# Kernel tuning notes

Hardware: AMD Instinct MI355X
Metric: run time of the kernel (lower is better)

## Reference

```python
import jax, jax.numpy as jnp
import numpy as np

N_NODES = 100000
N_EDGES = 3200000
IN_DIM = 256
HID_DIM = 64
OUT_DIM = 64


def setup_inputs() -> dict:
    key = jax.random.key(0)
    k1, k2, k3, k4, k5, k6 = jax.random.split(key, 6)
    x = jax.random.normal(k1, (N_NODES, IN_DIM), dtype=jnp.float32)
    edge_index = jax.random.randint(k2, (2, N_EDGES), 0, N_NODES, dtype=jnp.int32)
    # Glorot-style init for the two GCNConv layers (PyG default: glorot weight, zero bias)
    W1 = jax.random.normal(k3, (IN_DIM, HID_DIM), dtype=jnp.float32) * (1.0 / np.sqrt(IN_DIM))
    b1 = jnp.zeros((HID_DIM,), dtype=jnp.float32)
    W2 = jax.random.normal(k4, (HID_DIM, OUT_DIM), dtype=jnp.float32) * (1.0 / np.sqrt(HID_DIM))
    b2 = jnp.zeros((OUT_DIM,), dtype=jnp.float32)
    return {"x": x, "edge_index": edge_index, "W1": W1, "b1": b1, "W2": W2, "b2": b2}


def _gcn_conv(x, src, dst, deg_inv_sqrt, W, b, n):
    # PyG GCNConv: h = x W; out_i = sum_j norm_ij * h_j + b, with symmetric norm
    h = x @ W                                   # (n, d_out) small GEMM
    norm = deg_inv_sqrt[src] * deg_inv_sqrt[dst]  # (E+n,)
    msg = norm[:, None] * h[src]                # gather (E+n, d_out)
    agg = jax.ops.segment_sum(msg, dst, num_segments=n)  # scatter-add
    return agg + b


def reference(x, edge_index, W1, b1, W2, b2):
    n = x.shape[0]
    loops = jnp.arange(n, dtype=edge_index.dtype)
    src = jnp.concatenate([edge_index[0], loops])
    dst = jnp.concatenate([edge_index[1], loops])
    # degree on destination (col) with added self-loops, weight 1.0
    deg = jax.ops.segment_sum(jnp.ones_like(dst, dtype=x.dtype), dst, num_segments=n)
    deg_inv_sqrt = jnp.where(deg > 0, jax.lax.rsqrt(deg), 0.0)
    h = jax.nn.relu(_gcn_conv(x, src, dst, deg_inv_sqrt, W1, b1, n))
    return _gcn_conv(h, src, dst, deg_inv_sqrt, W2, b2, n)
```

## Files before the change

kernel.cpp:

```cpp
#include <hip/hip_runtime.h>
#include <cstdint>
#include <cstddef>


#define BIN_SHIFT 7
#define BIN_NODES 128
#define MAX_BINS 1024
#define SUP_SHIFT 11
#define FINE_PER_SUP 16
#define NSUP_MAX 64
#define SCAP 56
#define SRC_BITS 17
#define SRC_MASK ((1 << SRC_BITS) - 1)

typedef unsigned short ushort_t;

typedef __attribute__((ext_vector_type(8))) short bf16x8;
typedef __attribute__((ext_vector_type(4))) float f32x4;

union FragB {
  uint4 u;
  bf16x8 b;
};

__device__ __forceinline__ float4 bfq2f4(uint2 p) {
  float4 r;
  r.x = __uint_as_float(p.x << 16);
  r.y = __uint_as_float(p.x & 0xFFFF0000u);
  r.z = __uint_as_float(p.y << 16);
  r.w = __uint_as_float(p.y & 0xFFFF0000u);
  return r;
}
__device__ __forceinline__ unsigned f2bf(float f) {
  unsigned u = __float_as_uint(f);
  return (u + 0x7FFFu + ((u >> 16) & 1u)) >> 16;
}
__device__ __forceinline__ uint2 f42bfq(float4 f) {
  uint2 r;
  r.x = f2bf(f.x) | (f2bf(f.y) << 16);
  r.y = f2bf(f.z) | (f2bf(f.w) << 16);
  return r;
}

__global__ void zero_int(int* __restrict__ p, int n) {
  int i = blockIdx.x * blockDim.x + threadIdx.x;
  if (i < n) p[i] = 0;
}

__global__ __launch_bounds__(256) void bin_count(const int* __restrict__ dst, int E, int nbins,
                                                 int* __restrict__ binCnt) {
  __shared__ int h[MAX_BINS];
  for (int i = threadIdx.x; i < nbins; i += 256) h[i] = 0;
  __syncthreads();
  int stride = gridDim.x * 256;
  for (int e = blockIdx.x * 256 + threadIdx.x; e < E; e += stride)
    atomicAdd(&h[dst[e] >> BIN_SHIFT], 1);
  __syncthreads();
  for (int i = threadIdx.x; i < nbins; i += 256)
    if (h[i]) atomicAdd(&binCnt[i], h[i]);
}

__global__ __launch_bounds__(256) void bin_scan(const int* __restrict__ binCnt, int nbins, int E,
                                                int* __restrict__ binStart,
                                                int* __restrict__ binCursor,
                                                int* __restrict__ supCursor) {
  __shared__ int s[256];
  int t = threadIdx.x;
  int c[4];
  int sum = 0;
#pragma unroll
  for (int i = 0; i < 4; i++) {
    int idx = t * 4 + i;
    c[i] = (idx < nbins) ? binCnt[idx] : 0;
    sum += c[i];
  }
  int v = sum;
  s[t] = v;
  __syncthreads();
  for (int d = 1; d < 256; d <<= 1) {
    int add = (t >= d) ? s[t - d] : 0;
    __syncthreads();
    s[t] += add;
    __syncthreads();
  }
  int run = s[t] - v;
#pragma unroll
  for (int i = 0; i < 4; i++) {
    int idx = t * 4 + i;
    if (idx < nbins) {
      binStart[idx] = run;
      binCursor[idx] = run;
      if ((idx & (FINE_PER_SUP - 1)) == 0) supCursor[idx >> 4] = run;
      run += c[i];
    }
  }
  if (t == 0) binStart[nbins] = E;
}

__global__ __launch_bounds__(256) void super_fill(const int* __restrict__ src,
                                                  const int* __restrict__ dst, int E, int nsup,
                                                  int* __restrict__ supCursor,
                                                  unsigned* __restrict__ supbuf) {
  __shared__ unsigned stage[NSUP_MAX * SCAP];
  __shared__ int lcnt[NSUP_MAX], lbase[NSUP_MAX], lscan[NSUP_MAX + 1];
  const int tid = threadIdx.x;
  const int t0 = blockIdx.x * 2048;
  const int t1 = min(E, t0 + 2048);

  int dv[8], sv[8];
#pragma unroll
  for (int i = 0; i < 8; i++) {
    int e = t0 + i * 256 + tid;
    if (e < t1) {
      dv[i] = dst[e];
      sv[i] = src[e];
    }
  }
  if (tid < nsup) lcnt[tid] = 0;
  __syncthreads();
#pragma unroll
  for (int i = 0; i < 8; i++) {
    int e = t0 + i * 256 + tid;
    if (e < t1) {
      int d = dv[i];
      int sb = d >> SUP_SHIFT;
      unsigned v = ((unsigned)(d & ((1 << SUP_SHIFT) - 1)) << SRC_BITS) | (unsigned)sv[i];
      int idx = atomicAdd(&lcnt[sb], 1);
      if (idx < SCAP)
        stage[sb * SCAP + idx] = v;
      else {
        int g = atomicAdd(&supCursor[sb], 1);
        supbuf[g] = v;
      }
    }
  }
  __syncthreads();
  if (tid < nsup) {
    int c = min(lcnt[tid], SCAP);
    lcnt[tid] = c;
    lbase[tid] = c ? atomicAdd(&supCursor[tid], c) : 0;
  }
  __syncthreads();
  if (tid < 64) {
    int vv = (tid < nsup) ? lcnt[tid] : 0;
    int ss = vv;
#pragma unroll
    for (int d = 1; d < 64; d <<= 1) {
      int u = __shfl_up(ss, d);
      if (tid >= d) ss += u;
    }
    lscan[tid + 1] = ss;
    if (tid == 0) lscan[0] = 0;
  }
  __syncthreads();
  int total = lscan[nsup];
  for (int j = tid; j < total; j += 256) {
    int lo = 0, hi = nsup;
    while (hi - lo > 1) {
      int mid = (lo + hi) >> 1;
      if (lscan[mid] <= j)
        lo = mid;
      else
        hi = mid;
    }
    int off = j - lscan[lo];
    supbuf[lbase[lo] + off] = stage[lo * SCAP + off];
  }
}

__global__ __launch_bounds__(256) void fine_fill(const unsigned* __restrict__ supbuf,
                                                 const int* __restrict__ binStart, int nbins,
                                                 int* __restrict__ binCursor,
                                                 unsigned* __restrict__ binbuf) {
  __shared__ int lcnt[FINE_PER_SUP], lbase[FINE_PER_SUP];
  int sb = blockIdx.x >> 3, p = blockIdx.x & 7;
  int seg0 = binStart[sb << 4];
  int seg1 = binStart[min((sb + 1) << 4, nbins)];
  int part = (seg1 - seg0 + 7) >> 3;
  int c0 = seg0 + p * part;
  int c1 = min(seg1, c0 + part);
  if (threadIdx.x < FINE_PER_SUP) lcnt[threadIdx.x] = 0;
  __syncthreads();
  for (int i = c0 + threadIdx.x; i < c1; i += 256) atomicAdd(&lcnt[supbuf[i] >> 24], 1);
  __syncthreads();
  if (threadIdx.x < FINE_PER_SUP) {
    int c = lcnt[threadIdx.x];
    lbase[threadIdx.x] = c ? atomicAdd(&binCursor[(sb << 4) + threadIdx.x], c) : 0;
    lcnt[threadIdx.x] = 0;
  }
  __syncthreads();
  for (int i = c0 + threadIdx.x; i < c1; i += 256) {
    unsigned v = supbuf[i];
    unsigned dls = v >> SRC_BITS;
    int f = dls >> BIN_SHIFT;
    unsigned vf = ((dls & (BIN_NODES - 1)) << SRC_BITS) | (v & SRC_MASK);
    int idx = lbase[f] + atomicAdd(&lcnt[f], 1);
    binbuf[idx] = vf;
  }
}

__global__ __launch_bounds__(256) void node_count_dis(const unsigned* __restrict__ binbuf,
                                                      const int* __restrict__ binStart, int N,
                                                      int* __restrict__ count,
                                                      float* __restrict__ dis) {
  __shared__ int cnt[BIN_NODES];
  int b = blockIdx.x;
  int nodeBase = b << BIN_SHIFT;
  if (threadIdx.x < BIN_NODES) cnt[threadIdx.x] = 0;
  __syncthreads();
  int s0 = binStart[b], s1 = binStart[b + 1];
  for (int i = s0 + threadIdx.x; i < s1; i += 256) atomicAdd(&cnt[binbuf[i] >> SRC_BITS], 1);
  __syncthreads();
  if (threadIdx.x < BIN_NODES) {
    int node = nodeBase + threadIdx.x;
    if (node < N) {
      int c = cnt[threadIdx.x];
      count[node] = c;
      dis[node] = rsqrtf((float)(c + 1));
    }
  }
}

__global__ __launch_bounds__(256) void bin_csr(const unsigned* __restrict__ binbuf,
                                               const int* __restrict__ binStart,
                                               const int* __restrict__ count, int N, int E,
                                               int* __restrict__ rowptr, int* __restrict__ col) {
  __shared__ int cur[BIN_NODES];
  __shared__ int pref[BIN_NODES];
  int b = blockIdx.x, t = threadIdx.x;
  int nodeBase = b << BIN_SHIFT;
  int c = 0;
  if (t < BIN_NODES) {
    int node = nodeBase + t;
    c = (node < N) ? count[node] : 0;
    pref[t] = c;
  }
  __syncthreads();
  for (int d = 1; d < BIN_NODES; d <<= 1) {
    int add = (t < BIN_NODES && t >= d) ? pref[t - d] : 0;
    __syncthreads();
    if (t < BIN_NODES) pref[t] += add;
    __syncthreads();
  }
  int s0 = binStart[b];
  if (t < BIN_NODES) {
    int node = nodeBase + t;
    if (node < N) {
      int ex = s0 + pref[t] - c;
      rowptr[node] = ex;
      cur[t] = ex;
    }
  }
  if (b == 0 && t == 255) rowptr[N] = E;
  __syncthreads();
  int s1 = binStart[b + 1];
  for (int i = s0 + t; i < s1; i += 256) {
    unsigned v = binbuf[i];
    int slot = atomicAdd(&cur[v >> SRC_BITS], 1);
    col[slot] = v & SRC_MASK;
  }
}

__global__ __launch_bounds__(256) void wsplit(const float* __restrict__ W1,
                                              const float* __restrict__ W2,
                                              ushort_t* __restrict__ wt1,
                                              ushort_t* __restrict__ wt2) {
  int i = blockIdx.x * 256 + threadIdx.x;
  const float* W;
  ushort_t* wt;
  int K, idx;
  if (i < 256 * 64) {
    W = W1; wt = wt1; K = 256; idx = i;
  } else if (i < 256 * 64 + 64 * 64) {
    W = W2; wt = wt2; K = 64; idx = i - 256 * 64;
  } else
    return;
  int n = idx & 63, k = idx >> 6;
  float f = W[k * 64 + n];
  unsigned u = __float_as_uint(f);
  unsigned hb = u & 0xFFFF0000u;
  float lo = f - __uint_as_float(hb);
  wt[(size_t)n * K + k] = (ushort_t)(u >> 16);
  wt[(size_t)64 * K + (size_t)n * K + k] = (ushort_t)(__float_as_uint(lo) >> 16);
}

__device__ __forceinline__ void split8u(uint4 a, uint4 b, uint4& xh, uint4& xl) {
  unsigned ua[8] = {a.x, a.y, a.z, a.w, b.x, b.y, b.z, b.w};
  unsigned hw[4], lw[4];
#pragma unroll
  for (int p = 0; p < 4; p++) {
    unsigned u0 = ua[2 * p], u1 = ua[2 * p + 1];
    unsigned h0 = u0 & 0xFFFF0000u, h1 = u1 & 0xFFFF0000u;
    float l0 = __uint_as_float(u0) - __uint_as_float(h0);
    float l1 = __uint_as_float(u1) - __uint_as_float(h1);
    hw[p] = (u0 >> 16) | h1;
    lw[p] = (__float_as_uint(l0) >> 16) | (__float_as_uint(l1) & 0xFFFF0000u);
  }
  xh = make_uint4(hw[0], hw[1], hw[2], hw[3]);
  xl = make_uint4(lw[0], lw[1], lw[2], lw[3]);
}

__global__ __launch_bounds__(256, 3) void gemm1_mfma(const float* __restrict__ A,
                                                     const ushort_t* __restrict__ Wt,
                                                     uint2* __restrict__ Cb, int M) {
  constexpr int K = 256;
  __shared__ uint4 xtile[3][4][256];
  const int lane = threadIdx.x & 63;
  const int wv = threadIdx.x >> 6;
  const int l15 = lane & 15;
  const int lq = lane >> 4;
  const int m0 = blockIdx.x * 128 + wv * 32;

  const ushort_t* __restrict__ Wlo = Wt + (size_t)64 * K;

  f32x4 acc[2][4];
#pragma unroll
  for (int a = 0; a < 2; a++)
#pragma unroll
    for (int b = 0; b < 4; b++) acc[a][b] = (f32x4){0.f, 0.f, 0.f, 0.f};

  auto stage_tile = [&](int kt, int buf) {
#pragma unroll
    for (int c = 0; c < 4; c++) {
      int s = c * 64 + lane;
      int r = s >> 3;
      int c4 = (s & 7) ^ (r & 7);
      int nd = m0 + r;
      if (nd >= M) nd = M - 1;
      const float* gp = A + (size_t)nd * K + kt * 32 + c4 * 4;
      __builtin_amdgcn_global_load_lds(
          (const __attribute__((address_space(1))) void*)gp,
          (__attribute__((address_space(3))) void*)&xtile[buf][wv][c * 64], 16, 0, 0);
    }
  };
  auto load_w = [&](int kt, FragB* wr) {
    const int kb = kt * 32 + lq * 8;
#pragma unroll
    for (int nt = 0; nt < 4; nt++) {
      wr[nt].u = *(const uint4*)(Wt + (size_t)(nt * 16 + l15) * K + kb);
      wr[4 + nt].u = *(const uint4*)(Wlo + (size_t)(nt * 16 + l15) * K + kb);
    }
  };

  FragB w[2][8];
  stage_tile(0, 0);
  load_w(0, w[0]);
  __builtin_amdgcn_sched_barrier(0);
  stage_tile(1, 1);
  __builtin_amdgcn_sched_barrier(0);

#pragma unroll
  for (int j = 0; j < 8; j++) {
    if (j < 7)
      asm volatile("s_waitcnt vmcnt(12)" ::: "memory");
    else
      asm volatile("s_waitcnt vmcnt(8)" ::: "memory");
    __builtin_amdgcn_sched_barrier(0);
    uint4 xa[2][2];
#pragma unroll
    for (int mt = 0; mt < 2; mt++) {
      int mr = mt * 16 + l15;
#pragma unroll
      for (int hh = 0; hh < 2; hh++) {
        int c4 = (lq * 2 + hh) ^ (mr & 7);
        xa[mt][hh] = *(const uint4*)&xtile[j % 3][wv][mr * 8 + c4];
      }
    }
    if (j + 1 < 8) load_w(j + 1, w[(j + 1) & 1]);
    __builtin_amdgcn_sched_barrier(0);
    if (j + 2 < 8) stage_tile(j + 2, (j + 2) % 3);
    __builtin_amdgcn_sched_barrier(0);
    FragB xh0, xl0, xh1, xl1;
    split8u(xa[0][0], xa[0][1], xh0.u, xl0.u);
    split8u(xa[1][0], xa[1][1], xh1.u, xl1.u);
    const FragB* wc = w[j & 1];
#pragma unroll
    for (int nt = 0; nt < 4; nt++) {
      acc[0][nt] = __builtin_amdgcn_mfma_f32_16x16x32_bf16(wc[nt].b, xh0.b, acc[0][nt], 0, 0, 0);
      acc[0][nt] = __builtin_amdgcn_mfma_f32_16x16x32_bf16(wc[nt].b, xl0.b, acc[0][nt], 0, 0, 0);
      acc[1][nt] = __builtin_amdgcn_mfma_f32_16x16x32_bf16(wc[nt].b, xh1.b, acc[1][nt], 0, 0, 0);
      acc[1][nt] = __builtin_amdgcn_mfma_f32_16x16x32_bf16(wc[nt].b, xl1.b, acc[1][nt], 0, 0, 0);
    }
#pragma unroll
    for (int nt = 0; nt < 4; nt++) {
      acc[0][nt] = __builtin_amdgcn_mfma_f32_16x16x32_bf16(wc[4 + nt].b, xh0.b, acc[0][nt], 0, 0, 0);
      acc[1][nt] = __builtin_amdgcn_mfma_f32_16x16x32_bf16(wc[4 + nt].b, xh1.b, acc[1][nt], 0, 0, 0);
    }
  }

#pragma unroll
  for (int mt = 0; mt < 2; mt++) {
    int node = m0 + mt * 16 + l15;
    if (node < M) {
      uint2* cp = Cb + (size_t)node * 16 + lq;
#pragma unroll
      for (int nt = 0; nt < 4; nt++) {
        float4 o = make_float4(acc[mt][nt][0], acc[mt][nt][1], acc[mt][nt][2], acc[mt][nt][3]);
        cp[nt * 4] = f42bfq(o);
      }
    }
  }
}

__global__ __launch_bounds__(256, 3) void gemm2_mfma(const ushort_t* __restrict__ Av,
                                                     const ushort_t* __restrict__ Wt,
                                                     uint2* __restrict__ Cb, int M) {
  constexpr int K = 64;
  constexpr int NT = K / 32;
  const int lane = threadIdx.x & 63;
  const int wv = threadIdx.x >> 6;
  const int l15 = lane & 15;
  const int lq = lane >> 4;
  const int m0 = blockIdx.x * 128 + wv * 32;

  const ushort_t* __restrict__ Wlo = Wt + (size_t)64 * K;

  f32x4 acc[2][4];
#pragma unroll
  for (int a = 0; a < 2; a++)
#pragma unroll
    for (int b = 0; b < 4; b++) acc[a][b] = (f32x4){0.f, 0.f, 0.f, 0.f};

  int node[2], ncl[2];
#pragma unroll
  for (int mt = 0; mt < 2; mt++) {
    node[mt] = m0 + mt * 16 + l15;
    ncl[mt] = node[mt] < M ? node[mt] : (M - 1);
  }

  FragB xa[NT][2], wh[NT][4], wl[NT][4];
#pragma unroll
  for (int t = 0; t < NT; t++)
#pragma unroll
    for (int mt = 0; mt < 2; mt++)
      xa[t][mt].u = *(const uint4*)(Av + (size_t)ncl[mt] * K + t * 32 + lq * 8);
#pragma unroll
  for (int t = 0; t < NT; t++)
#pragma unroll
    for (int nt = 0; nt < 4; nt++) {
      wh[t][nt].u = *(const uint4*)(Wt + (size_t)(nt * 16 + l15) * K + t * 32 + lq * 8);
      wl[t][nt].u = *(const uint4*)(Wlo + (size_t)(nt * 16 + l15) * K + t * 32 + lq * 8);
    }
#pragma unroll
  for (int t = 0; t < NT; t++)
#pragma unroll
    for (int mt = 0; mt < 2; mt++)
#pragma unroll
      for (int nt = 0; nt < 4; nt++) {
        acc[mt][nt] =
            __builtin_amdgcn_mfma_f32_16x16x32_bf16(wh[t][nt].b, xa[t][mt].b, acc[mt][nt], 0, 0, 0);
        acc[mt][nt] =
            __builtin_amdgcn_mfma_f32_16x16x32_bf16(wl[t][nt].b, xa[t][mt].b, acc[mt][nt], 0, 0, 0);
      }

#pragma unroll
  for (int mt = 0; mt < 2; mt++) {
    if (node[mt] < M) {
      uint2* cp = Cb + (size_t)node[mt] * 16 + lq;
#pragma unroll
      for (int nt = 0; nt < 4; nt++) {
        float4 o = make_float4(acc[mt][nt][0], acc[mt][nt][1], acc[mt][nt][2], acc[mt][nt][3]);
        cp[nt * 4] = f42bfq(o);
      }
    }
  }
}

template <bool OUTBF>
__global__ __launch_bounds__(256) void agg_kernel(
    const uint2* __restrict__ h, const int* __restrict__ rowptr, const int* __restrict__ col,
    const float* __restrict__ dis, const float* __restrict__ bias, void* __restrict__ outv,
    int N, int relu) {
  int wid = (blockIdx.x * blockDim.x + threadIdx.x) >> 6;
  if (wid >= N) return;
  int lane = threadIdx.x & 63;
  int sub = lane & 15;
  int quarter = lane >> 4;

  int start = rowptr[wid], end = rowptr[wid + 1];
  float di = dis[wid];

  float4 a0 = make_float4(0.f, 0.f, 0.f, 0.f), a1 = a0, a2 = a0, a3 = a0;
  {
    float4 self = bfq2f4(h[(size_t)wid * 16 + sub]);
    if (quarter == 0) {
      a0.x = di * self.x;
      a0.y = di * self.y;
      a0.z = di * self.z;
      a0.w = di * self.w;
    }
  }

  for (int base = start; base < end; base += 64) {
    int e = base + lane;
    int sj = 0;
    float wj = 0.f;
    if (e < end) {
      sj = col[e];
      wj = dis[sj];
    }
    int cnt = end - base;
    if (cnt > 64) cnt = 64;
    int rounds = (cnt + 3) >> 2;
    int t = 0;
    for (; t + 4 <= rounds; t += 4) {
      int i0 = 4 * t + quarter;
      int s0 = __shfl(sj, i0), s1 = __shfl(sj, i0 + 4), s2 = __shfl(sj, i0 + 8),
          s3 = __shfl(sj, i0 + 12);
      float w0 = __shfl(wj, i0), w1 = __shfl(wj, i0 + 4), w2 = __shfl(wj, i0 + 8),
            w3 = __shfl(wj, i0 + 12);
      float4 g0 = bfq2f4(h[(size_t)s0 * 16 + sub]);
      float4 g1 = bfq2f4(h[(size_t)s1 * 16 + sub]);
      float4 g2 = bfq2f4(h[(size_t)s2 * 16 + sub]);
      float4 g3 = bfq2f4(h[(size_t)s3 * 16 + sub]);
      a0.x += w0 * g0.x; a0.y += w0 * g0.y; a0.z += w0 * g0.z; a0.w += w0 * g0.w;
      a1.x += w1 * g1.x; a1.y += w1 * g1.y; a1.z += w1 * g1.z; a1.w += w1 * g1.w;
      a2.x += w2 * g2.x; a2.y += w2 * g2.y; a2.z += w2 * g2.z; a2.w += w2 * g2.w;
      a3.x += w3 * g3.x; a3.y += w3 * g3.y; a3.z += w3 * g3.z; a3.w += w3 * g3.w;
    }
    for (; t < rounds; t++) {
      int i0 = 4 * t + quarter;
      int s0 = __shfl(sj, i0);
      float w0 = __shfl(wj, i0);
      float4 g0 = bfq2f4(h[(size_t)s0 * 16 + sub]);
      a0.x += w0 * g0.x; a0.y += w0 * g0.y; a0.z += w0 * g0.z; a0.w += w0 * g0.w;
    }
  }

  float sx = (a0.x + a1.x) + (a2.x + a3.x);
  float sy = (a0.y + a1.y) + (a2.y + a3.y);
  float sz = (a0.z + a1.z) + (a2.z + a3.z);
  float sw = (a0.w + a1.w) + (a2.w + a3.w);
  sx += __shfl_down(sx, 32); sy += __shfl_down(sy, 32);
  sz += __shfl_down(sz, 32); sw += __shfl_down(sw, 32);
  sx += __shfl_down(sx, 16); sy += __shfl_down(sy, 16);
  sz += __shfl_down(sz, 16); sw += __shfl_down(sw, 16);
  if (quarter == 0) {
    float4 bv = ((const float4*)bias)[sub];
    float4 o = make_float4(di * sx + bv.x, di * sy + bv.y, di * sz + bv.z, di * sw + bv.w);
    if (relu) {
      o.x = fmaxf(o.x, 0.f);
      o.y = fmaxf(o.y, 0.f);
      o.z = fmaxf(o.z, 0.f);
      o.w = fmaxf(o.w, 0.f);
    }
    if (OUTBF)
      ((uint2*)outv)[(size_t)wid * 16 + sub] = f42bfq(o);
    else
      ((float4*)outv)[(size_t)wid * 16 + sub] = o;
  }
}

extern "C" void kernel_launch(void* const* d_in, const int* in_sizes, int n_in,
                              void* d_out, int out_size, void* d_ws, size_t ws_size,
                              hipStream_t stream) {
  const float* x = (const float*)d_in[0];
  const int* ei = (const int*)d_in[1];
  const float* W1 = (const float*)d_in[2];
  const float* b1 = (const float*)d_in[3];
  const float* W2 = (const float*)d_in[4];
  const float* b2 = (const float*)d_in[5];

  const int IN = 256;
  const int E = in_sizes[1] / 2;
  const int N = in_sizes[0] / IN;
  const int* src = ei;
  const int* dst = ei + E;
  const int nbins = (N + BIN_NODES - 1) >> BIN_SHIFT;
  const int nsup = (N + (1 << SUP_SHIFT) - 1) >> SUP_SHIFT;

  char* ws = (char*)d_ws;
  size_t off = 0;
  auto alloc = [&](size_t bytes) -> void* {
    void* p = ws + off;
    off += (bytes + 255) & ~(size_t)255;
    return p;
  };
  int* count = (int*)alloc((size_t)N * 4);
  int* rowptr = (int*)alloc((size_t)(N + 1) * 4);
  float* dis = (float*)alloc((size_t)N * 4);
  int* binCnt = (int*)alloc(MAX_BINS * 4);
  int* binStart = (int*)alloc((MAX_BINS + 1) * 4);
  int* binCursor = (int*)alloc(MAX_BINS * 4);
  int* supCursor = (int*)alloc(NSUP_MAX * 4);
  int* col = (int*)alloc((size_t)E * 4);
  unsigned* supbuf = (unsigned*)col;
  uint2* out1 = (uint2*)alloc((size_t)N * 64 * 2);
  size_t big = ((size_t)E * 4 > (size_t)N * 128) ? (size_t)E * 4 : (size_t)N * 128;
  unsigned* binbuf = (unsigned*)alloc(big);
  uint2* h = (uint2*)binbuf;
  ushort_t* wt1 = (ushort_t*)alloc((size_t)2 * 64 * 256 * 2);
  ushort_t* wt2 = (ushort_t*)alloc((size_t)2 * 64 * 64 * 2);
  float* outf = (float*)d_out;

  zero_int<<<(nbins + 255) / 256, 256, 0, stream>>>(binCnt, nbins);
  bin_count<<<1024, 256, 0, stream>>>(dst, E, nbins, binCnt);
  bin_scan<<<1, 256, 0, stream>>>(binCnt, nbins, E, binStart, binCursor, supCursor);
  super_fill<<<(E + 2047) / 2048, 256, 0, stream>>>(src, dst, E, nsup, supCursor, supbuf);
  fine_fill<<<nsup * 8, 256, 0, stream>>>(supbuf, binStart, nbins, binCursor, binbuf);
  node_count_dis<<<nbins, 256, 0, stream>>>(binbuf, binStart, N, count, dis);
  bin_csr<<<nbins, 256, 0, stream>>>(binbuf, binStart, count, N, E, rowptr, col);
  wsplit<<<(256 * 64 + 64 * 64 + 255) / 256, 256, 0, stream>>>(W1, W2, wt1, wt2);

  gemm1_mfma<<<(N + 127) / 128, 256, 0, stream>>>(x, wt1, h, N);
  agg_kernel<true><<<(N + 3) / 4, 256, 0, stream>>>(h, rowptr, col, dis, b1, out1, N, 1);
  gemm2_mfma<<<(N + 127) / 128, 256, 0, stream>>>((const ushort_t*)out1, wt2, h, N);
  agg_kernel<false><<<(N + 3) / 4, 256, 0, stream>>>(h, rowptr, col, dis, b2, outf, N, 0);
}
```

Measured before the change: 463.6 us.

## Process four nodes per wavefront in aggregation and load GEMM1 weights inline

The aggregation kernel now assigns four consecutive destination nodes to each wavefront, preloading their rowptr and dis values and the bias, and launches a quarter as many blocks. This is meant to amortise per-wave setup and scheduling overhead, at the cost of fewer waves in flight to hide gather latency and more serial work per wave. GEMM1 also drops its double-buffered weight-fragment prefetch and loads the weight fragments inside each k-step, tightening the vmcnt waits. That lowers register use but exposes weight-load latency in every iteration.

After: 473.2 us. 2.1% more time.

```diff
diff --git a/kernel.cpp b/kernel.cpp
--- a/kernel.cpp
+++ b/kernel.cpp
@@ -333,29 +333,27 @@
           (__attribute__((address_space(3))) void*)&xtile[buf][wv][c * 64], 16, 0, 0);
     }
   };
-  auto load_w = [&](int kt, FragB* wr) {
-    const int kb = kt * 32 + lq * 8;
-#pragma unroll
-    for (int nt = 0; nt < 4; nt++) {
-      wr[nt].u = *(const uint4*)(Wt + (size_t)(nt * 16 + l15) * K + kb);
-      wr[4 + nt].u = *(const uint4*)(Wlo + (size_t)(nt * 16 + l15) * K + kb);
-    }
-  };
-
-  FragB w[2][8];
+
   stage_tile(0, 0);
-  load_w(0, w[0]);
-  __builtin_amdgcn_sched_barrier(0);
   stage_tile(1, 1);
   __builtin_amdgcn_sched_barrier(0);
 
 #pragma unroll
   for (int j = 0; j < 8; j++) {
     if (j < 7)
-      asm volatile("s_waitcnt vmcnt(12)" ::: "memory");
+      asm volatile("s_waitcnt vmcnt(4)" ::: "memory");
     else
-      asm volatile("s_waitcnt vmcnt(8)" ::: "memory");
+      asm volatile("s_waitcnt vmcnt(0)" ::: "memory");
     __builtin_amdgcn_sched_barrier(0);
+    FragB w[8];
+    {
+      const int kb = j * 32 + lq * 8;
+#pragma unroll
+      for (int nt = 0; nt < 4; nt++) {
+        w[nt].u = *(const uint4*)(Wt + (size_t)(nt * 16 + l15) * K + kb);
+        w[4 + nt].u = *(const uint4*)(Wlo + (size_t)(nt * 16 + l15) * K + kb);
+      }
+    }
     uint4 xa[2][2];
 #pragma unroll
     for (int mt = 0; mt < 2; mt++) {
@@ -366,25 +364,23 @@
         xa[mt][hh] = *(const uint4*)&xtile[j % 3][wv][mr * 8 + c4];
       }
     }
-    if (j + 1 < 8) load_w(j + 1, w[(j + 1) & 1]);
     __builtin_amdgcn_sched_barrier(0);
     if (j + 2 < 8) stage_tile(j + 2, (j + 2) % 3);
     __builtin_amdgcn_sched_barrier(0);
     FragB xh0, xl0, xh1, xl1;
     split8u(xa[0][0], xa[0][1], xh0.u, xl0.u);
     split8u(xa[1][0], xa[1][1], xh1.u, xl1.u);
-    const FragB* wc = w[j & 1];
 #pragma unroll
     for (int nt = 0; nt < 4; nt++) {
-      acc[0][nt] = __builtin_amdgcn_mfma_f32_16x16x32_bf16(wc[nt].b, xh0.b, acc[0][nt], 0, 0, 0);
-      acc[0][nt] = __builtin_amdgcn_mfma_f32_16x16x32_bf16(wc[nt].b, xl0.b, acc[0][nt], 0, 0, 0);
-      acc[1][nt] = __builtin_amdgcn_mfma_f32_16x16x32_bf16(wc[nt].b, xh1.b, acc[1][nt], 0, 0, 0);
-      acc[1][nt] = __builtin_amdgcn_mfma_f32_16x16x32_bf16(wc[nt].b, xl1.b, acc[1][nt], 0, 0, 0);
+      acc[0][nt] = __builtin_amdgcn_mfma_f32_16x16x32_bf16(w[nt].b, xh0.b, acc[0][nt], 0, 0, 0);
+      acc[0][nt] = __builtin_amdgcn_mfma_f32_16x16x32_bf16(w[nt].b, xl0.b, acc[0][nt], 0, 0, 0);
+      acc[1][nt] = __builtin_amdgcn_mfma_f32_16x16x32_bf16(w[nt].b, xh1.b, acc[1][nt], 0, 0, 0);
+      acc[1][nt] = __builtin_amdgcn_mfma_f32_16x16x32_bf16(w[nt].b, xl1.b, acc[1][nt], 0, 0, 0);
     }
 #pragma unroll
     for (int nt = 0; nt < 4; nt++) {
-      acc[0][nt] = __builtin_amdgcn_mfma_f32_16x16x32_bf16(wc[4 + nt].b, xh0.b, acc[0][nt], 0, 0, 0);
-      acc[1][nt] = __builtin_amdgcn_mfma_f32_16x16x32_bf16(wc[4 + nt].b, xh1.b, acc[1][nt], 0, 0, 0);
+      acc[0][nt] = __builtin_amdgcn_mfma_f32_16x16x32_bf16(w[4 + nt].b, xh0.b, acc[0][nt], 0, 0, 0);
+      acc[1][nt] = __builtin_amdgcn_mfma_f32_16x16x32_bf16(w[4 + nt].b, xh1.b, acc[1][nt], 0, 0, 0);
     }
   }
 
@@ -471,83 +467,96 @@
     const uint2* __restrict__ h, const int* __restrict__ rowptr, const int* __restrict__ col,
     const float* __restrict__ dis, const float* __restrict__ bias, void* __restrict__ outv,
     int N, int relu) {
-  int wid = (blockIdx.x * blockDim.x + threadIdx.x) >> 6;
-  if (wid >= N) return;
+  int wq = (blockIdx.x * blockDim.x + threadIdx.x) >> 6;
+  int n0 = wq * 4;
+  if (n0 >= N) return;
   int lane = threadIdx.x & 63;
   int sub = lane & 15;
   int quarter = lane >> 4;
 
-  int start = rowptr[wid], end = rowptr[wid + 1];
-  float di = dis[wid];
-
-  float4 a0 = make_float4(0.f, 0.f, 0.f, 0.f), a1 = a0, a2 = a0, a3 = a0;
-  {
-    float4 self = bfq2f4(h[(size_t)wid * 16 + sub]);
+  int rp[5];
+  float dd[4];
+#pragma unroll
+  for (int i = 0; i < 5; i++) rp[i] = rowptr[min(n0 + i, N)];
+#pragma unroll
+  for (int i = 0; i < 4; i++) dd[i] = (n0 + i < N) ? dis[n0 + i] : 0.f;
+  float4 bv = ((const float4*)bias)[sub];
+
+#pragma unroll
+  for (int ni = 0; ni < 4; ni++) {
+    int wid = n0 + ni;
+    if (wid >= N) break;
+    int start = rp[ni], end = rp[ni + 1];
+    float di = dd[ni];
+
+    float4 a0 = make_float4(0.f, 0.f, 0.f, 0.f), a1 = a0, a2 = a0, a3 = a0;
+    {
+      float4 self = bfq2f4(h[(size_t)wid * 16 + sub]);
+      if (quarter == 0) {
+        a0.x = di * self.x;
+        a0.y = di * self.y;
+        a0.z = di * self.z;
+        a0.w = di * self.w;
+      }
+    }
+
+    for (int base = start; base < end; base += 64) {
+      int e = base + lane;
+      int sj = 0;
+      float wj = 0.f;
+      if (e < end) {
+        sj = col[e];
+        wj = dis[sj];
+      }
+      int cnt = end - base;
+      if (cnt > 64) cnt = 64;
+      int rounds = (cnt + 3) >> 2;
+      int t = 0;
+      for (; t + 4 <= rounds; t += 4) {
+        int i0 = 4 * t + quarter;
+        int s0 = __shfl(sj, i0), s1 = __shfl(sj, i0 + 4), s2 = __shfl(sj, i0 + 8),
+            s3 = __shfl(sj, i0 + 12);
+        float w0 = __shfl(wj, i0), w1 = __shfl(wj, i0 + 4), w2 = __shfl(wj, i0 + 8),
+              w3 = __shfl(wj, i0 + 12);
+        float4 g0 = bfq2f4(h[(size_t)s0 * 16 + sub]);
+        float4 g1 = bfq2f4(h[(size_t)s1 * 16 + sub]);
+        float4 g2 = bfq2f4(h[(size_t)s2 * 16 + sub]);
+        float4 g3 = bfq2f4(h[(size_t)s3 * 16 + sub]);
+        a0.x += w0 * g0.x; a0.y += w0 * g0.y; a0.z += w0 * g0.z; a0.w += w0 * g0.w;
+        a1.x += w1 * g1.x; a1.y += w1 * g1.y; a1.z += w1 * g1.z; a1.w += w1 * g1.w;
+        a2.x += w2 * g2.x; a2.y += w2 * g2.y; a2.z += w2 * g2.z; a2.w += w2 * g2.w;
+        a3.x += w3 * g3.x; a3.y += w3 * g3.y; a3.z += w3 * g3.z; a3.w += w3 * g3.w;
+      }
+      for (; t < rounds; t++) {
+        int i0 = 4 * t + quarter;
+        int s0 = __shfl(sj, i0);
+        float w0 = __shfl(wj, i0);
+        float4 g0 = bfq2f4(h[(size_t)s0 * 16 + sub]);
+        a0.x += w0 * g0.x; a0.y += w0 * g0.y; a0.z += w0 * g0.z; a0.w += w0 * g0.w;
+      }
+    }
+
+    float sx = (a0.x + a1.x) + (a2.x + a3.x);
+    float sy = (a0.y + a1.y) + (a2.y + a3.y);
+    float sz = (a0.z + a1.z) + (a2.z + a3.z);
+    float sw = (a0.w + a1.w) + (a2.w + a3.w);
+    sx += __shfl_down(sx, 32); sy += __shfl_down(sy, 32);
+    sz += __shfl_down(sz, 32); sw += __shfl_down(sw, 32);
+    sx += __shfl_down(sx, 16); sy += __shfl_down(sy, 16);
+    sz += __shfl_down(sz, 16); sw += __shfl_down(sw, 16);
     if (quarter == 0) {
-      a0.x = di * self.x;
-      a0.y = di * self.y;
-      a0.z = di * self.z;
-      a0.w = di * self.w;
-    }
-  }
-
-  for (int base = start; base < end; base += 64) {
-    int e = base + lane;
-    int sj = 0;
-    float wj = 0.f;
-    if (e < end) {
-      sj = col[e];
-      wj = dis[sj];
-    }
-    int cnt = end - base;
-    if (cnt > 64) cnt = 64;
-    int rounds = (cnt + 3) >> 2;
-    int t = 0;
-    for (; t + 4 <= rounds; t += 4) {
-      int i0 = 4 * t + quarter;
-      int s0 = __shfl(sj, i0), s1 = __shfl(sj, i0 + 4), s2 = __shfl(sj, i0 + 8),
-          s3 = __shfl(sj, i0 + 12);
-      float w0 = __shfl(wj, i0), w1 = __shfl(wj, i0 + 4), w2 = __shfl(wj, i0 + 8),
-            w3 = __shfl(wj, i0 + 12);
-      float4 g0 = bfq2f4(h[(size_t)s0 * 16 + sub]);
-      float4 g1 = bfq2f4(h[(size_t)s1 * 16 + sub]);
-      float4 g2 = bfq2f4(h[(size_t)s2 * 16 + sub]);
-      float4 g3 = bfq2f4(h[(size_t)s3 * 16 + sub]);
-      a0.x += w0 * g0.x; a0.y += w0 * g0.y; a0.z += w0 * g0.z; a0.w += w0 * g0.w;
-      a1.x += w1 * g1.x; a1.y += w1 * g1.y; a1.z += w1 * g1.z; a1.w += w1 * g1.w;
-      a2.x += w2 * g2.x; a2.y += w2 * g2.y; a2.z += w2 * g2.z; a2.w += w2 * g2.w;
-      a3.x += w3 * g3.x; a3.y += w3 * g3.y; a3.z += w3 * g3.z; a3.w += w3 * g3.w;
-    }
-    for (; t < rounds; t++) {
-      int i0 = 4 * t + quarter;
-      int s0 = __shfl(sj, i0);
-      float w0 = __shfl(wj, i0);
-      float4 g0 = bfq2f4(h[(size_t)s0 * 16 + sub]);
-      a0.x += w0 * g0.x; a0.y += w0 * g0.y; a0.z += w0 * g0.z; a0.w += w0 * g0.w;
-    }
-  }
-
-  float sx = (a0.x + a1.x) + (a2.x + a3.x);
-  float sy = (a0.y + a1.y) + (a2.y + a3.y);
-  float sz = (a0.z + a1.z) + (a2.z + a3.z);
-  float sw = (a0.w + a1.w) + (a2.w + a3.w);
-  sx += __shfl_down(sx, 32); sy += __shfl_down(sy, 32);
-  sz += __shfl_down(sz, 32); sw += __shfl_down(sw, 32);
-  sx += __shfl_down(sx, 16); sy += __shfl_down(sy, 16);
-  sz += __shfl_down(sz, 16); sw += __shfl_down(sw, 16);
-  if (quarter == 0) {
-    float4 bv = ((const float4*)bias)[sub];
-    float4 o = make_float4(di * sx + bv.x, di * sy + bv.y, di * sz + bv.z, di * sw + bv.w);
-    if (relu) {
-      o.x = fmaxf(o.x, 0.f);
-      o.y = fmaxf(o.y, 0.f);
-      o.z = fmaxf(o.z, 0.f);
-      o.w = fmaxf(o.w, 0.f);
-    }
-    if (OUTBF)
-      ((uint2*)outv)[(size_t)wid * 16 + sub] = f42bfq(o);
-    else
-      ((float4*)outv)[(size_t)wid * 16 + sub] = o;
+      float4 o = make_float4(di * sx + bv.x, di * sy + bv.y, di * sz + bv.z, di * sw + bv.w);
+      if (relu) {
+        o.x = fmaxf(o.x, 0.f);
+        o.y = fmaxf(o.y, 0.f);
+        o.z = fmaxf(o.z, 0.f);
+        o.w = fmaxf(o.w, 0.f);
+      }
+      if (OUTBF)
+        ((uint2*)outv)[(size_t)wid * 16 + sub] = f42bfq(o);
+      else
+        ((float4*)outv)[(size_t)wid * 16 + sub] = o;
+    }
   }
 }
 
@@ -603,7 +612,7 @@
   wsplit<<<(256 * 64 + 64 * 64 + 255) / 256, 256, 0, stream>>>(W1, W2, wt1, wt2);
 
   gemm1_mfma<<<(N + 127) / 128, 256, 0, stream>>>(x, wt1, h, N);
-  agg_kernel<true><<<(N + 3) / 4, 256, 0, stream>>>(h, rowptr, col, dis, b1, out1, N, 1);
+  agg_kernel<true><<<(N + 15) / 16, 256, 0, stream>>>(h, rowptr, col, dis, b1, out1, N, 1);
   gemm2_mfma<<<(N + 127) / 128, 256, 0, stream>>>((const ushort_t*)out1, wt2, h, N);
-  agg_kernel<false><<<(N + 3) / 4, 256, 0, stream>>>(h, rowptr, col, dis, b2, outf, N, 0);
-}
+  agg_kernel<false><<<(N + 15) / 16, 256, 0, stream>>>(h, rowptr, col, dis, b2, outf, N, 0);
+}
```
